# Performance work log

Hardware: AMD Instinct MI355X
Metric: run time of the kernel (lower is better)

The kernel has to match this reference:

```python
import jax, jax.numpy as jnp
import numpy as np


def _mlp3(x, w0, b0, w1, b1, w2, b2):
    x = jax.nn.relu(x @ w0.T + b0)
    x = jax.nn.relu(x @ w1.T + b1)
    return x @ w2.T + b2


def setup_inputs() -> dict:
    key = jax.random.key(0)
    ks = jax.random.split(key, 32)
    B, T, C, E, H, A = 64, 256, 53, 64, 64, 128
    C2 = C * C
    s = 0.1  # weight scale for numerical stability
    inp = {
        'x': jax.random.normal(ks[0], (B, T, C), jnp.float32),
        'w_emb': s * jax.random.normal(ks[1], (E, 1), jnp.float32),
        'b_emb': s * jax.random.normal(ks[2], (E,), jnp.float32),
        'w_ih': s * jax.random.normal(ks[3], (3 * H, E), jnp.float32),
        'w_hh': s * jax.random.normal(ks[4], (3 * H, H), jnp.float32),
        'b_ih': s * jax.random.normal(ks[5], (3 * H,), jnp.float32),
        'b_hh': s * jax.random.normal(ks[6], (3 * H,), jnp.float32),
        'q_w0': s * jax.random.normal(ks[7], (A, H), jnp.float32),
        'q_b0': s * jax.random.normal(ks[8], (A,), jnp.float32),
        'q_w1': s * jax.random.normal(ks[9], (A, A), jnp.float32),
        'q_b1': s * jax.random.normal(ks[10], (A,), jnp.float32),
        'q_w2': s * jax.random.normal(ks[11], (A, A), jnp.float32),
        'q_b2': s * jax.random.normal(ks[12], (A,), jnp.float32),
        'k_w0': s * jax.random.normal(ks[13], (A, H), jnp.float32),
        'k_b0': s * jax.random.normal(ks[14], (A,), jnp.float32),
        'k_w1': s * jax.random.normal(ks[15], (A, A), jnp.float32),
        'k_b1': s * jax.random.normal(ks[16], (A,), jnp.float32),
        'k_w2': s * jax.random.normal(ks[17], (A, A), jnp.float32),
        'k_b2': s * jax.random.normal(ks[18], (A,), jnp.float32),
        'gate_bias': jax.random.normal(ks[19], (C, C), jnp.float32),
        'pred_w': s * jax.random.normal(ks[20], (1, H), jnp.float32),
        'pred_b': s * jax.random.normal(ks[21], (1,), jnp.float32),
        'clf_w0': 0.02 * jax.random.normal(ks[22], (C2 // 2, C2), jnp.float32),
        'clf_b0': s * jax.random.normal(ks[23], (C2 // 2,), jnp.float32),
        'clf_w1': 0.02 * jax.random.normal(ks[24], (C2 // 4, C2 // 2), jnp.float32),
        'clf_b1': s * jax.random.normal(ks[25], (C2 // 4,), jnp.float32),
        'clf_w2': 0.02 * jax.random.normal(ks[26], (2, C2 // 4), jnp.float32),
        'clf_b2': s * jax.random.normal(ks[27], (2,), jnp.float32),
    }
    return inp


def reference(x, w_emb, b_emb, w_ih, w_hh, b_ih, b_hh,
              q_w0, q_b0, q_w1, q_b1, q_w2, q_b2,
              k_w0, k_b0, k_w1, k_b1, k_w2, k_b2,
              gate_bias, pred_w, pred_b,
              clf_w0, clf_b0, clf_w1, clf_b1, clf_w2, clf_b2):
    B, T, C = x.shape
    H = w_hh.shape[1]
    # single_embed Linear(1, E): embedded[b,t,c,e] = x[b,t,c]*w[e] + b[e]
    embedded = x[..., None] * w_emb[:, 0] + b_emb          # (B,T,C,E)
    emb_t = jnp.transpose(embedded, (1, 0, 2, 3))           # (T,B,C,E)
    h0 = jnp.zeros((B, C, H), x.dtype)

    def step(h, e_t):
        # GRU cell over B*C independent sequences (vectorized as (B,C,*))
        gi = e_t @ w_ih.T + b_ih                            # (B,C,3H)
        gh = h @ w_hh.T + b_hh
        ir, iz, inn = jnp.split(gi, 3, axis=-1)
        hr, hz, hn = jnp.split(gh, 3, axis=-1)
        r = jax.nn.sigmoid(ir + hr)
        z = jax.nn.sigmoid(iz + hz)
        n = jnp.tanh(inn + r * hn)
        h_gru = (1.0 - z) * n + z * h                       # (B,C,H)
        # gated self-attention mixing across components
        q = _mlp3(h_gru, q_w0, q_b0, q_w1, q_b1, q_w2, q_b2)
        k = _mlp3(h_gru, k_w0, k_b0, k_w1, k_b1, k_w2, k_b2)
        transfer = jnp.einsum('bch,bdh->bcd', q, k)         # (B,C,C)
        norms = jnp.sqrt(jnp.sum(transfer * transfer, axis=(1, 2), keepdims=True))
        transfer = transfer / norms                         # Frobenius matrix-norm divide
        gate = jax.nn.sigmoid(jnp.abs(transfer) + gate_bias)
        transfer = transfer * gate
        h_new = jnp.einsum('bcd,bdh->bch', transfer, h_gru)
        return h_new, (h_new, transfer)

    _, (hs, mix) = jax.lax.scan(step, h0, emb_t)
    hs = jnp.transpose(hs, (1, 0, 2, 3))                    # (B,T,C,H)
    mix = jnp.transpose(mix, (1, 0, 2, 3))                  # (B,T,C,C)

    hidden = hs[:, :-1]                                     # (B,T-1,C,H)
    predicted = (hidden @ pred_w.T + pred_b)[..., 0]        # (B,T-1,C)

    clf_in = mix.reshape(B, T, -1)                          # (B,T,C^2)
    mean_FNC = jnp.mean(clf_in, axis=1).reshape(B, C, C)
    z1 = jax.nn.relu(clf_in @ clf_w0.T + clf_b0)            # dropout is identity (eval)
    z2 = jax.nn.relu(z1 @ clf_w1.T + clf_b1)
    logits = jnp.mean(z2 @ clf_w2.T + clf_b2, axis=1)       # (B,2)
    return (logits, mean_FNC, mix, predicted, x[:, 1:, :])
```

## Files before the change

kernel.cpp:

```cpp
#include <hip/hip_runtime.h>
#include <hip/hip_fp16.h>

typedef _Float16 f16;
typedef f16 f16x4 __attribute__((ext_vector_type(4)));
typedef f16 f16x8 __attribute__((ext_vector_type(8)));
typedef float f32x4 __attribute__((ext_vector_type(4)));
typedef float f32x4u __attribute__((ext_vector_type(4), aligned(4)));

#define DEVINL __device__ __forceinline__
#define MFMA16(a, b, c) __builtin_amdgcn_mfma_f32_16x16x32_f16(a, b, c, 0, 0, 0)

#define BARRIER_LDS() asm volatile("s_waitcnt lgkmcnt(0)\n\ts_barrier" ::: "memory")

DEVINL float sigmoidf_(float v) { return 1.f / (1.f + __expf(-v)); }


__global__ __launch_bounds__(512)
void scan_kernel(const float* __restrict__ x,
                 const float* __restrict__ w_emb,
                 const float* __restrict__ b_emb,
                 const float* __restrict__ w_ih,
                 const float* __restrict__ w_hh,
                 const float* __restrict__ b_ih,
                 const float* __restrict__ b_hh,
                 const float* __restrict__ qw0, const float* __restrict__ qb0,
                 const float* __restrict__ qw1, const float* __restrict__ qb1,
                 const float* __restrict__ qw2, const float* __restrict__ qb2,
                 const float* __restrict__ kw0, const float* __restrict__ kb0,
                 const float* __restrict__ kw1, const float* __restrict__ kb1,
                 const float* __restrict__ kw2, const float* __restrict__ kb2,
                 const float* __restrict__ gate_bias,
                 const float* __restrict__ pred_w,
                 const float* __restrict__ pred_b,
                 float* __restrict__ out_meanF,
                 float* __restrict__ out_mix,
                 float* __restrict__ out_pred,
                 float* __restrict__ out_xcopy)
{
    __shared__ __align__(16) unsigned char smem[64900];
    float* hh  = (float*)smem;
    f16*   hK  = (f16*)(smem + 15232);
    f16*   hC  = (f16*)(smem + 23424);
    f16*   qk0 = (f16*)(smem + 31616);
    f16*   qk1 = (f16*)(smem + 48000);
    f16*   gh  = (f16*)(smem + 31616);
    f16*   trK = (f16*)(smem + 31616);
    float* xc  = (float*)(smem + 64384);
    float* pw  = (float*)(smem + 64608);
    float* red = (float*)(smem + 64864);

    const int b    = blockIdx.x;
    const int tid  = threadIdx.x;
    const int wv   = tid >> 6;
    const int lane = tid & 63;
    const int quad = lane >> 4;
    const int l15  = lane & 15;
    const int colg = (wv << 3) + (lane >> 3);
    const int rsub = lane & 7;

#define FRAG(buf, kt, nt) ((buf) + ((((kt) * 4 + (nt)) * 64 + lane) * 8))

    for (int i = tid; i < 56 * 68; i += 512) hh[i] = 0.f;
    for (int i = tid; i < 4096; i += 512) { hK[i] = (f16)0.f; hC[i] = (f16)0.f; }
    if (tid < 56) xc[tid] = 0.f;
    if (tid < 64) pw[tid] = pred_w[tid];

    float a_r = 0.f, a_z = 0.f, a_n = 0.f, s_r = 0.f, s_z = 0.f, s_n = 0.f;
    for (int e = 0; e < 64; e++) {
        float we = w_emb[e], be = b_emb[e];
        float w0 = w_ih[colg * 64 + e];
        float w1 = w_ih[(64 + colg) * 64 + e];
        float w2 = w_ih[(128 + colg) * 64 + e];
        a_r += w0 * we; s_r += w0 * be;
        a_z += w1 * we; s_z += w1 * be;
        a_n += w2 * we; s_n += w2 * be;
    }
    const float c_r = s_r + b_ih[colg] + b_hh[colg];
    const float c_z = s_z + b_ih[64 + colg] + b_hh[64 + colg];
    const float c_n = s_n + b_ih[128 + colg];
    const float bhn = b_hh[128 + colg];
    const float pb  = pred_b[0];

    auto ldfrag = [&](const float* W, int K, int mt, int kt) -> f16x8 {
        const float* p = W + (size_t)(mt * 16 + l15) * K + kt * 32 + quad * 8;
        float4 u0 = *(const float4*)p;
        float4 u1 = *(const float4*)(p + 4);
        f16x8 a;
        a[0] = (f16)u0.x; a[1] = (f16)u0.y; a[2] = (f16)u0.z; a[3] = (f16)u0.w;
        a[4] = (f16)u1.x; a[5] = (f16)u1.y; a[6] = (f16)u1.z; a[7] = (f16)u1.w;
        return a;
    };

    const int mtLo = (6 * wv) >> 2, mtHi = (6 * wv + 5) >> 2;
    f16x8 wg0k0 = ldfrag(w_hh, 64, mtLo, 0), wg0k1 = ldfrag(w_hh, 64, mtLo, 1);
    f16x8 wg1k0 = ldfrag(w_hh, 64, mtHi, 0), wg1k1 = ldfrag(w_hh, 64, mtHi, 1);

    f16x8 wq0f[2], wk0f[2], wq1f[4], wq2f[4], wk1f[4], wk2f[4];
#pragma unroll
    for (int kt = 0; kt < 2; kt++) {
        wq0f[kt] = ldfrag(qw0, 64, wv, kt);
        wk0f[kt] = ldfrag(kw0, 64, wv, kt);
    }
#pragma unroll
    for (int kt = 0; kt < 4; kt++) {
        wq1f[kt] = ldfrag(qw1, 128, wv, kt);
        wq2f[kt] = ldfrag(qw2, 128, wv, kt);
        wk1f[kt] = ldfrag(kw1, 128, wv, kt);
        wk2f[kt] = ldfrag(kw2, 128, wv, kt);
    }

    const int f0 = wv * 16 + quad * 4;
    f32x4 bq0v, bq1v, bq2v, bk0v, bk1v, bk2v;
#pragma unroll
    for (int r = 0; r < 4; r++) {
        bq0v[r] = qb0[f0 + r]; bq1v[r] = qb1[f0 + r]; bq2v[r] = qb2[f0 + r];
        bk0v[r] = kb0[f0 + r]; bk1v[r] = kb1[f0 + r]; bk2v[r] = kb2[f0 + r];
    }

    const int tmt = wv & 3, tnt0 = (wv >> 2) * 2;
    float gbv[8], mf[8];
#pragma unroll
    for (int i = 0; i < 2; i++)
#pragma unroll
        for (int r = 0; r < 4; r++) {
            int c = tmt * 16 + quad * 4 + r, d = (tnt0 + i) * 16 + l15;
            gbv[i * 4 + r] = (c < 53 && d < 53) ? gate_bias[c * 53 + d] : 0.f;
            mf[i * 4 + r] = 0.f;
        }

    auto cwrite = [&](f16* dst, int ct, const f32x4 acc, const f32x4 bv, bool rel) {
        const int kts  = wv >> 1;
        const int sub  = (2 * wv + (quad >> 1)) & 3;
        const int base = ((kts * 4 + ct) * 64 + (l15 + 16 * sub)) * 8 + (quad & 1) * 4;
        f16x4 pk;
#pragma unroll
        for (int r = 0; r < 4; r++) {
            float v = acc[r] + bv[r];
            if (rel) v = fmaxf(v, 0.f);
            pk[r] = (f16)v;
        }
        *(f16x4*)(dst + base) = pk;
    };

    __syncthreads();

    f16x8 bf[4][4];

#define PRELOAD(SRC) do { \
    _Pragma("unroll") for (int ct = 0; ct < 4; ct++) \
        _Pragma("unroll") for (int kt = 0; kt < 4; kt++) \
            bf[ct][kt] = *(const f16x8*)FRAG(SRC, kt, ct); } while (0)

#define MLP4(WF, DST, BV, REL) do { \
    f32x4 a0 = {0.f,0.f,0.f,0.f}, a1 = {0.f,0.f,0.f,0.f}; \
    f32x4 a2 = {0.f,0.f,0.f,0.f}, a3 = {0.f,0.f,0.f,0.f}; \
    _Pragma("unroll") for (int kt = 0; kt < 4; kt++) { \
        a0 = MFMA16(WF[kt], bf[0][kt], a0); \
        a1 = MFMA16(WF[kt], bf[1][kt], a1); \
        a2 = MFMA16(WF[kt], bf[2][kt], a2); \
        a3 = MFMA16(WF[kt], bf[3][kt], a3); } \
    cwrite(DST, 0, a0, BV, REL); cwrite(DST, 1, a1, BV, REL); \
    cwrite(DST, 2, a2, BV, REL); cwrite(DST, 3, a3, BV, REL); } while (0)

    float xv = 0.f;
    if (tid < 53) xv = x[(size_t)b * 256 * 53 + tid];

    for (int t = 0; t < 256; t++) {
        if (tid < 53) xc[tid] = xv;
        {
#pragma unroll
            for (int i = 0; i < 6; i++) {
                int tau = 6 * wv + i, mt = tau >> 2, ct = tau & 3;
                bool hi = (mt != mtLo);
                f32x4 acc = {0.f, 0.f, 0.f, 0.f};
                acc = MFMA16(hi ? wg1k0 : wg0k0, *(const f16x8*)FRAG(hK, 0, ct), acc);
                acc = MFMA16(hi ? wg1k1 : wg0k1, *(const f16x8*)FRAG(hK, 1, ct), acc);
                int gbase = (mt * 16 + quad * 4) * 68 + ct * 16 + l15;
#pragma unroll
                for (int r = 0; r < 4; r++) gh[gbase + r * 68] = (f16)acc[r];
            }
        }
        BARRIER_LDS();
        {
#pragma unroll
            for (int r = 0; r < 7; r++) {
                int c = rsub + 8 * r;
                float hr = (float)gh[colg * 68 + c];
                float hz = (float)gh[(64 + colg) * 68 + c];
                float hn = (float)gh[(128 + colg) * 68 + c];
                float xcv = xc[c];
                float hp = hh[c * 68 + colg];
                float rr = sigmoidf_(xcv * a_r + c_r + hr);
                float zz = sigmoidf_(xcv * a_z + c_z + hz);
                float e2 = __expf(2.f * (xcv * a_n + c_n + rr * (hn + bhn)));
                float nn = 1.f - 2.f / (e2 + 1.f);
                float hg = (1.f - zz) * nn + zz * hp;
                hh[c * 68 + colg] = hg;
                f16 h6 = (f16)hg;
                hK[(((colg >> 5) * 4 + (c >> 4)) * 64 + (c & 15) + 16 * ((colg >> 3) & 3)) * 8 + (colg & 7)] = h6;
                hC[(((c >> 5) * 4 + (colg >> 4)) * 64 + (colg & 15) + 16 * ((c >> 3) & 3)) * 8 + (c & 7)] = h6;
            }
        }
        BARRIER_LDS();
        {
            if (tid < 53) {
                if (t >= 1) out_xcopy[((size_t)b * 255 + (t - 1)) * 53 + tid] = xv;
                if (t < 255) xv = x[((size_t)b * 256 + t + 1) * 53 + tid];
            }
            f32x4 a0 = {0.f,0.f,0.f,0.f}, a1 = {0.f,0.f,0.f,0.f};
            f32x4 a2 = {0.f,0.f,0.f,0.f}, a3 = {0.f,0.f,0.f,0.f};
#pragma unroll
            for (int kt = 0; kt < 2; kt++) {
                a0 = MFMA16(wq0f[kt], *(const f16x8*)FRAG(hK, kt, 0), a0);
                a1 = MFMA16(wq0f[kt], *(const f16x8*)FRAG(hK, kt, 1), a1);
                a2 = MFMA16(wq0f[kt], *(const f16x8*)FRAG(hK, kt, 2), a2);
                a3 = MFMA16(wq0f[kt], *(const f16x8*)FRAG(hK, kt, 3), a3);
            }
            cwrite(qk0, 0, a0, bq0v, true); cwrite(qk0, 1, a1, bq0v, true);
            cwrite(qk0, 2, a2, bq0v, true); cwrite(qk0, 3, a3, bq0v, true);
            f32x4 k0 = {0.f,0.f,0.f,0.f}, k1 = {0.f,0.f,0.f,0.f};
            f32x4 k2 = {0.f,0.f,0.f,0.f}, k3 = {0.f,0.f,0.f,0.f};
#pragma unroll
            for (int kt = 0; kt < 2; kt++) {
                k0 = MFMA16(wk0f[kt], *(const f16x8*)FRAG(hK, kt, 0), k0);
                k1 = MFMA16(wk0f[kt], *(const f16x8*)FRAG(hK, kt, 1), k1);
                k2 = MFMA16(wk0f[kt], *(const f16x8*)FRAG(hK, kt, 2), k2);
                k3 = MFMA16(wk0f[kt], *(const f16x8*)FRAG(hK, kt, 3), k3);
            }
            cwrite(qk1, 0, k0, bk0v, true); cwrite(qk1, 1, k1, bk0v, true);
            cwrite(qk1, 2, k2, bk0v, true); cwrite(qk1, 3, k3, bk0v, true);
        }
        BARRIER_LDS();
        PRELOAD(qk0);
        BARRIER_LDS();
        MLP4(wq1f, qk0, bq1v, true);
        PRELOAD(qk1);
        BARRIER_LDS();
        MLP4(wk1f, qk1, bk1v, true);
        PRELOAD(qk0);
        BARRIER_LDS();
        MLP4(wq2f, qk0, bq2v, false);
        PRELOAD(qk1);
        BARRIER_LDS();
        MLP4(wk2f, qk1, bk2v, false);
        BARRIER_LDS();
        f32x4 tacc0 = {0.f,0.f,0.f,0.f}, tacc1 = {0.f,0.f,0.f,0.f};
        {
            f16x8 qa[4];
#pragma unroll
            for (int kt = 0; kt < 4; kt++) qa[kt] = *(const f16x8*)FRAG(qk0, kt, tmt);
#pragma unroll
            for (int kt = 0; kt < 4; kt++) {
                tacc0 = MFMA16(qa[kt], *(const f16x8*)FRAG(qk1, kt, tnt0), tacc0);
                tacc1 = MFMA16(qa[kt], *(const f16x8*)FRAG(qk1, kt, tnt0 + 1), tacc1);
            }
            float ssq = 0.f;
#pragma unroll
            for (int r = 0; r < 4; r++) {
                int c = tmt * 16 + quad * 4 + r;
                if (c < 53) {
                    if (tnt0 * 16 + l15 < 53)       ssq += tacc0[r] * tacc0[r];
                    if ((tnt0 + 1) * 16 + l15 < 53) ssq += tacc1[r] * tacc1[r];
                }
            }
#pragma unroll
            for (int off = 32; off > 0; off >>= 1) ssq += __shfl_down(ssq, off);
            if (lane == 0) red[wv] = ssq;
        }
        BARRIER_LDS();
        float ov[8];
        {
            float s2 = 0.f;
#pragma unroll
            for (int w8 = 0; w8 < 8; w8++) s2 += red[w8];
            const float inv = rsqrtf(s2);
#pragma unroll
            for (int i = 0; i < 2; i++)
#pragma unroll
                for (int r = 0; r < 4; r++) {
                    int c = tmt * 16 + quad * 4 + r;
                    int d = (tnt0 + i) * 16 + l15;
                    float v = (i == 0 ? tacc0[r] : tacc1[r]) * inv;
                    float g = sigmoidf_(fabsf(v) + gbv[i * 4 + r]);
                    v *= g;
                    bool ok = (c < 53) & (d < 53);
                    v = ok ? v : 0.f;
                    ov[i * 4 + r] = v;
                    mf[i * 4 + r] += v;
                    trK[(((d >> 5) * 4 + (c >> 4)) * 64 + (c & 15) + 16 * ((d >> 3) & 3)) * 8 + (d & 7)] = (f16)v;
                }
        }
        BARRIER_LDS();
        {
            const size_t mixbase = ((size_t)b * 256 + t) * 2809;
#pragma unroll
            for (int i = 0; i < 2; i++)
#pragma unroll
                for (int r = 0; r < 4; r++) {
                    int c = tmt * 16 + quad * 4 + r;
                    int d = (tnt0 + i) * 16 + l15;
                    if ((c < 53) & (d < 53)) out_mix[mixbase + c * 53 + d] = ov[i * 4 + r];
                }
        }
        {
            f32x4 h0 = {0.f,0.f,0.f,0.f}, h1 = {0.f,0.f,0.f,0.f};
            f16x8 ta0 = *(const f16x8*)FRAG(trK, 0, tmt);
            f16x8 ta1 = *(const f16x8*)FRAG(trK, 1, tmt);
            h0 = MFMA16(ta0, *(const f16x8*)FRAG(hC, 0, tnt0), h0);
            h0 = MFMA16(ta1, *(const f16x8*)FRAG(hC, 1, tnt0), h0);
            h1 = MFMA16(ta0, *(const f16x8*)FRAG(hC, 0, tnt0 + 1), h1);
            h1 = MFMA16(ta1, *(const f16x8*)FRAG(hC, 1, tnt0 + 1), h1);
#pragma unroll
            for (int i = 0; i < 2; i++)
#pragma unroll
                for (int r = 0; r < 4; r++) {
                    int c = tmt * 16 + quad * 4 + r;
                    int e = (tnt0 + i) * 16 + l15;
                    float v = (i == 0 ? h0[r] : h1[r]);
                    if (c < 56) hh[c * 68 + e] = v;
                    hK[(((e >> 5) * 4 + (c >> 4)) * 64 + (c & 15) + 16 * ((e >> 3) & 3)) * 8 + (e & 7)] = (f16)v;
                }
        }
        BARRIER_LDS();
        if (t < 255 && tid < 53) {
            const float* hrow = hh + tid * 68;
            float s = pb;
#pragma unroll 4
            for (int e4 = 0; e4 < 16; e4++) {
                float4 hv = *(const float4*)(hrow + e4 * 4);
                float4 wv4 = *(const float4*)(pw + e4 * 4);
                s += hv.x * wv4.x + hv.y * wv4.y + hv.z * wv4.z + hv.w * wv4.w;
            }
            out_pred[((size_t)b * 255 + t) * 53 + tid] = s;
        }
    }

#pragma unroll
    for (int i = 0; i < 2; i++)
#pragma unroll
        for (int r = 0; r < 4; r++) {
            int c = tmt * 16 + quad * 4 + r;
            int d = (tnt0 + i) * 16 + l15;
            if (c < 53 && d < 53)
                out_meanF[(size_t)b * 2809 + c * 53 + d] = mf[i * 4 + r] * (1.f / 256.f);
        }
#undef FRAG
#undef PRELOAD
#undef MLP4
}

DEVINL void cvt16(const float* p, f16x8& lo, f16x8& hi) {
    f32x4u u0 = *(const f32x4u*)p;
    f32x4u u1 = *(const f32x4u*)(p + 4);
    f32x4u u2 = *(const f32x4u*)(p + 8);
    f32x4u u3 = *(const f32x4u*)(p + 12);
    lo[0] = (f16)u0.x; lo[1] = (f16)u0.y; lo[2] = (f16)u0.z; lo[3] = (f16)u0.w;
    lo[4] = (f16)u1.x; lo[5] = (f16)u1.y; lo[6] = (f16)u1.z; lo[7] = (f16)u1.w;
    hi[0] = (f16)u2.x; hi[1] = (f16)u2.y; hi[2] = (f16)u2.z; hi[3] = (f16)u2.w;
    hi[4] = (f16)u3.x; hi[5] = (f16)u3.y; hi[6] = (f16)u3.z; hi[7] = (f16)u3.w;
}

template<bool AHALF, bool COLSUM>
__global__ __launch_bounds__(256)
void clf_mfma(const void* __restrict__ Ap,
              const float* __restrict__ W,
              const float* __restrict__ bias,
              __half* __restrict__ z_out,
              float* __restrict__ colsum_out,
              int N, int K, int lda, int Kpad, int ldz)
{
    __shared__ __align__(16) f16 As[4096];
    __shared__ __align__(16) f16 Bs[4096];

    const int tid  = threadIdx.x;
    const int wv   = tid >> 6;
    const int lane = tid & 63;
    const int quad = lane >> 4;
    const int l15  = lane & 15;
    const int wm   = wv & 1;
    const int wn   = wv >> 1;
    const int m0   = blockIdx.x * 128;
    const int n0   = blockIdx.y * 128;

    const int srow = tid >> 1;
    const int skh  = (tid & 1) * 16;
    const int sdst = ((srow >> 4) * 64 + (skh >> 3) * 16 + (srow & 15)) * 8;

    f32x4 acc[4][4];
#pragma unroll
    for (int i = 0; i < 4; i++)
#pragma unroll
        for (int j = 0; j < 4; j++)
            acc[i][j] = (f32x4){0.f, 0.f, 0.f, 0.f};

    for (int k0 = 0; k0 < Kpad; k0 += 32) {
        {
            f16x8 lo, hi;
            if constexpr (AHALF) {
                const f16* p = (const f16*)Ap + (size_t)(m0 + srow) * lda + k0 + skh;
                lo = *(const f16x8*)p;
                hi = *(const f16x8*)(p + 8);
            } else {
                const float* p = (const float*)Ap + (size_t)(m0 + srow) * lda + k0 + skh;
                if (k0 + 32 <= K) {
                    cvt16(p, lo, hi);
                } else {
                    int kr = K - (k0 + skh);
#pragma unroll
                    for (int j = 0; j < 8; j++) lo[j] = (f16)((j < kr) ? p[j] : 0.f);
#pragma unroll
                    for (int j = 0; j < 8; j++) hi[j] = (f16)((j + 8 < kr) ? p[j + 8] : 0.f);
                }
            }
            *(f16x8*)(As + sdst)       = lo;
            *(f16x8*)(As + sdst + 128) = hi;
        }
        {
            f16x8 lo, hi;
#pragma unroll
            for (int j = 0; j < 8; j++) { lo[j] = (f16)0.f; hi[j] = (f16)0.f; }
            const int nrow = n0 + srow;
            if (nrow < N) {
                const float* p = W + (size_t)nrow * K + k0 + skh;
                if (k0 + 32 <= K) {
                    cvt16(p, lo, hi);
                } else {
                    int kr = K - (k0 + skh);
#pragma unroll
                    for (int j = 0; j < 8; j++) lo[j] = (f16)((j < kr) ? p[j] : 0.f);
#pragma unroll
                    for (int j = 0; j < 8; j++) hi[j] = (f16)((j + 8 < kr) ? p[j + 8] : 0.f);
                }
            }
            *(f16x8*)(Bs + sdst)       = lo;
            *(f16x8*)(Bs + sdst + 128) = hi;
        }
        __syncthreads();
        {
            f16x8 afr[4], bfr[4];
#pragma unroll
            for (int i = 0; i < 4; i++)
                afr[i] = *(const f16x8*)(As + ((wm * 4 + i) * 64 + lane) * 8);
#pragma unroll
            for (int i = 0; i < 4; i++)
                bfr[i] = *(const f16x8*)(Bs + ((wn * 4 + i) * 64 + lane) * 8);
#pragma unroll
            for (int mi = 0; mi < 4; mi++)
#pragma unroll
                for (int ni = 0; ni < 4; ni++)
                    acc[mi][ni] = MFMA16(afr[mi], bfr[ni], acc[mi][ni]);
        }
        __syncthreads();
    }

    if constexpr (!COLSUM) {
#pragma unroll
        for (int ni = 0; ni < 4; ni++) {
            int n = n0 + wn * 64 + ni * 16 + l15;
            float bj = (n < N) ? bias[n] : 0.f;
#pragma unroll
            for (int mi = 0; mi < 4; mi++) {
                int m = m0 + wm * 64 + mi * 16 + quad * 4;
#pragma unroll
                for (int r = 0; r < 4; r++) {
                    float v = (n < N) ? fmaxf(acc[mi][ni][r] + bj, 0.f) : 0.f;
                    z_out[(size_t)(m + r) * ldz + n] = __float2half(v);
                }
            }
        }
    } else {
        const int batch = m0 >> 8;
#pragma unroll
        for (int ni = 0; ni < 4; ni++) {
            int n = n0 + wn * 64 + ni * 16 + l15;
            float bj = (n < N) ? bias[n] : 0.f;
            float s = 0.f;
#pragma unroll
            for (int mi = 0; mi < 4; mi++)
#pragma unroll
                for (int r = 0; r < 4; r++)
                    s += fmaxf(acc[mi][ni][r] + bj, 0.f);
            s += __shfl_down(s, 32);
            s += __shfl_down(s, 16);
            if (quad == 0 && n < N)
                atomicAdd(&colsum_out[batch * 704 + n], s);
        }
    }
}

__global__ __launch_bounds__(128)
void logits_kernel(const float* __restrict__ zsum,
                   const float* __restrict__ w2,
                   const float* __restrict__ b2,
                   float* __restrict__ out)
{
    int tid = threadIdx.x;
    int bb = tid >> 1, o = tid & 1;
    const float* zs = zsum + bb * 704;
    const float* wrow = w2 + o * 702;
    float s = 0.f;
    for (int j = 0; j < 702; j++) s += zs[j] * wrow[j];
    out[bb * 2 + o] = s * (1.f / 256.f) + b2[o];
}

extern "C" void kernel_launch(void* const* d_in, const int* in_sizes, int n_in,
                              void* d_out, int out_size, void* d_ws, size_t ws_size,
                              hipStream_t stream)
{
    const float* x      = (const float*)d_in[0];
    const float* w_emb  = (const float*)d_in[1];
    const float* b_emb  = (const float*)d_in[2];
    const float* w_ih   = (const float*)d_in[3];
    const float* w_hh   = (const float*)d_in[4];
    const float* b_ih   = (const float*)d_in[5];
    const float* b_hh   = (const float*)d_in[6];
    const float* qw0 = (const float*)d_in[7];
    const float* qb0 = (const float*)d_in[8];
    const float* qw1 = (const float*)d_in[9];
    const float* qb1 = (const float*)d_in[10];
    const float* qw2 = (const float*)d_in[11];
    const float* qb2 = (const float*)d_in[12];
    const float* kw0 = (const float*)d_in[13];
    const float* kb0 = (const float*)d_in[14];
    const float* kw1 = (const float*)d_in[15];
    const float* kb1 = (const float*)d_in[16];
    const float* kw2 = (const float*)d_in[17];
    const float* kb2 = (const float*)d_in[18];
    const float* gate_bias = (const float*)d_in[19];
    const float* pred_w = (const float*)d_in[20];
    const float* pred_b = (const float*)d_in[21];
    const float* cw0 = (const float*)d_in[22];
    const float* cb0 = (const float*)d_in[23];
    const float* cw1 = (const float*)d_in[24];
    const float* cb1 = (const float*)d_in[25];
    const float* cw2 = (const float*)d_in[26];
    const float* cb2 = (const float*)d_in[27];

    float* out_logits = (float*)d_out;
    float* out_meanF  = (float*)d_out + 128;
    float* out_mix    = (float*)d_out + 128 + 179776;
    float* out_pred   = out_mix + 46022656;
    float* out_xcopy  = out_pred + 864960;

    float*  zsum = (float*)d_ws;
    __half* z1   = (__half*)((char*)d_ws + (1 << 18));

    hipMemsetAsync(zsum, 0, 64 * 704 * sizeof(float), stream);

    scan_kernel<<<64, 512, 0, stream>>>(
        x, w_emb, b_emb, w_ih, w_hh, b_ih, b_hh,
        qw0, qb0, qw1, qb1, qw2, qb2,
        kw0, kb0, kw1, kb1, kw2, kb2,
        gate_bias, pred_w, pred_b,
        out_meanF, out_mix, out_pred, out_xcopy);

    clf_mfma<false, false><<<dim3(128, 11), 256, 0, stream>>>(
        out_mix, cw0, cb0, z1, nullptr, 1404, 2809, 2809, 2816, 1408);

    clf_mfma<true, true><<<dim3(128, 6), 256, 0, stream>>>(
        z1, cw1, cb1, nullptr, zsum, 702, 1404, 1408, 1408, 0);

    logits_kernel<<<1, 128, 0, stream>>>(zsum, cw2, cb2, out_logits);
}
```

Baseline: 3.103 ms.

## Emit fp16 padded mix copy from scan and register-prefetch GEMM tiles

The scan kernel now also writes an fp16 copy of the mix matrix into workspace, padded to a 2816-element row stride with zeroed tail columns. When the workspace is large enough, the first classifier GEMM reads this half-precision copy with aligned vector loads instead of converting fp32 mix rows. The GEMM kernel also gains a software pipeline that loads the next K-tile into registers while the current tile is computed, and swaps __syncthreads for an lgkmcnt wait plus barrier. The cost is extra global writes in the serial scan kernel and a larger workspace requirement.

```diff
diff --git a/kernel.cpp b/kernel.cpp
--- a/kernel.cpp
+++ b/kernel.cpp
@@ -35,7 +35,8 @@
                  float* __restrict__ out_meanF,
                  float* __restrict__ out_mix,
                  float* __restrict__ out_pred,
-                 float* __restrict__ out_xcopy)
+                 float* __restrict__ out_xcopy,
+                 f16* __restrict__ out_mixh)
 {
     __shared__ __align__(16) unsigned char smem[64900];
     float* hh  = (float*)smem;
@@ -64,6 +65,12 @@
     for (int i = tid; i < 4096; i += 512) { hK[i] = (f16)0.f; hC[i] = (f16)0.f; }
     if (tid < 56) xc[tid] = 0.f;
     if (tid < 64) pw[tid] = pred_w[tid];
+    if (out_mixh) {
+        for (int i = tid; i < 256 * 7; i += 512) {
+            int row = b * 256 + i / 7, cc = 2809 + i % 7;
+            out_mixh[(size_t)row * 2816 + cc] = (f16)0.f;
+        }
+    }
 
     float a_r = 0.f, a_z = 0.f, a_n = 0.f, s_r = 0.f, s_z = 0.f, s_n = 0.f;
     for (int e = 0; e < 64; e++) {
@@ -293,13 +300,18 @@
         BARRIER_LDS();
         {
             const size_t mixbase = ((size_t)b * 256 + t) * 2809;
+            const size_t mhbase  = ((size_t)b * 256 + t) * 2816;
 #pragma unroll
             for (int i = 0; i < 2; i++)
 #pragma unroll
                 for (int r = 0; r < 4; r++) {
                     int c = tmt * 16 + quad * 4 + r;
                     int d = (tnt0 + i) * 16 + l15;
-                    if ((c < 53) & (d < 53)) out_mix[mixbase + c * 53 + d] = ov[i * 4 + r];
+                    if ((c < 53) & (d < 53)) {
+                        float v = ov[i * 4 + r];
+                        out_mix[mixbase + c * 53 + d] = v;
+                        if (out_mixh) out_mixh[mhbase + c * 53 + d] = (f16)v;
+                    }
                 }
         }
         {
@@ -347,17 +359,6 @@
 #undef FRAG
 #undef PRELOAD
 #undef MLP4
-}
-
-DEVINL void cvt16(const float* p, f16x8& lo, f16x8& hi) {
-    f32x4u u0 = *(const f32x4u*)p;
-    f32x4u u1 = *(const f32x4u*)(p + 4);
-    f32x4u u2 = *(const f32x4u*)(p + 8);
-    f32x4u u3 = *(const f32x4u*)(p + 12);
-    lo[0] = (f16)u0.x; lo[1] = (f16)u0.y; lo[2] = (f16)u0.z; lo[3] = (f16)u0.w;
-    lo[4] = (f16)u1.x; lo[5] = (f16)u1.y; lo[6] = (f16)u1.z; lo[7] = (f16)u1.w;
-    hi[0] = (f16)u2.x; hi[1] = (f16)u2.y; hi[2] = (f16)u2.z; hi[3] = (f16)u2.w;
-    hi[4] = (f16)u3.x; hi[5] = (f16)u3.y; hi[6] = (f16)u3.z; hi[7] = (f16)u3.w;
 }
 
 template<bool AHALF, bool COLSUM>
@@ -385,6 +386,8 @@
     const int srow = tid >> 1;
     const int skh  = (tid & 1) * 16;
     const int sdst = ((srow >> 4) * 64 + (skh >> 3) * 16 + (srow & 15)) * 8;
+    const int nrow = n0 + srow;
+    const bool bok = (nrow < N);
 
     f32x4 acc[4][4];
 #pragma unroll
@@ -393,49 +396,73 @@
         for (int j = 0; j < 4; j++)
             acc[i][j] = (f32x4){0.f, 0.f, 0.f, 0.f};
 
-    for (int k0 = 0; k0 < Kpad; k0 += 32) {
-        {
+    f16x8 pa0, pa1;
+    float fa[16];
+    float fb[16];
+
+    auto issueA = [&](int k0) {
+        if constexpr (AHALF) {
+            const f16* p = (const f16*)Ap + (size_t)(m0 + srow) * lda + k0 + skh;
+            pa0 = *(const f16x8*)p;
+            pa1 = *(const f16x8*)(p + 8);
+        } else {
+            const float* p = (const float*)Ap + (size_t)(m0 + srow) * lda + k0 + skh;
+            if (k0 + 32 <= K) {
+#pragma unroll
+                for (int q4 = 0; q4 < 4; q4++) {
+                    f32x4u u = *(const f32x4u*)(p + q4 * 4);
+                    fa[q4 * 4] = u[0]; fa[q4 * 4 + 1] = u[1];
+                    fa[q4 * 4 + 2] = u[2]; fa[q4 * 4 + 3] = u[3];
+                }
+            } else {
+#pragma unroll
+                for (int j = 0; j < 16; j++) {
+                    int k = k0 + skh + j;
+                    fa[j] = (k < K) ? p[j] : 0.f;
+                }
+            }
+        }
+    };
+    auto issueB = [&](int k0) {
+        const float* p = W + (size_t)nrow * K + k0 + skh;
+        if (bok && k0 + 32 <= K) {
+#pragma unroll
+            for (int q4 = 0; q4 < 4; q4++) {
+                f32x4u u = *(const f32x4u*)(p + q4 * 4);
+                fb[q4 * 4] = u[0]; fb[q4 * 4 + 1] = u[1];
+                fb[q4 * 4 + 2] = u[2]; fb[q4 * 4 + 3] = u[3];
+            }
+        } else {
+#pragma unroll
+            for (int j = 0; j < 16; j++) {
+                int k = k0 + skh + j;
+                fb[j] = (bok && k < K) ? p[j] : 0.f;
+            }
+        }
+    };
+    auto stage = [&]() {
+        if constexpr (AHALF) {
+            *(f16x8*)(As + sdst)       = pa0;
+            *(f16x8*)(As + sdst + 128) = pa1;
+        } else {
             f16x8 lo, hi;
-            if constexpr (AHALF) {
-                const f16* p = (const f16*)Ap + (size_t)(m0 + srow) * lda + k0 + skh;
-                lo = *(const f16x8*)p;
-                hi = *(const f16x8*)(p + 8);
-            } else {
-                const float* p = (const float*)Ap + (size_t)(m0 + srow) * lda + k0 + skh;
-                if (k0 + 32 <= K) {
-                    cvt16(p, lo, hi);
-                } else {
-                    int kr = K - (k0 + skh);
-#pragma unroll
-                    for (int j = 0; j < 8; j++) lo[j] = (f16)((j < kr) ? p[j] : 0.f);
-#pragma unroll
-                    for (int j = 0; j < 8; j++) hi[j] = (f16)((j + 8 < kr) ? p[j + 8] : 0.f);
-                }
-            }
+#pragma unroll
+            for (int j = 0; j < 8; j++) { lo[j] = (f16)fa[j]; hi[j] = (f16)fa[j + 8]; }
             *(f16x8*)(As + sdst)       = lo;
             *(f16x8*)(As + sdst + 128) = hi;
         }
-        {
-            f16x8 lo, hi;
-#pragma unroll
-            for (int j = 0; j < 8; j++) { lo[j] = (f16)0.f; hi[j] = (f16)0.f; }
-            const int nrow = n0 + srow;
-            if (nrow < N) {
-                const float* p = W + (size_t)nrow * K + k0 + skh;
-                if (k0 + 32 <= K) {
-                    cvt16(p, lo, hi);
-                } else {
-                    int kr = K - (k0 + skh);
-#pragma unroll
-                    for (int j = 0; j < 8; j++) lo[j] = (f16)((j < kr) ? p[j] : 0.f);
-#pragma unroll
-                    for (int j = 0; j < 8; j++) hi[j] = (f16)((j + 8 < kr) ? p[j + 8] : 0.f);
-                }
-            }
-            *(f16x8*)(Bs + sdst)       = lo;
-            *(f16x8*)(Bs + sdst + 128) = hi;
-        }
-        __syncthreads();
+        f16x8 blo, bhi;
+#pragma unroll
+        for (int j = 0; j < 8; j++) { blo[j] = (f16)fb[j]; bhi[j] = (f16)fb[j + 8]; }
+        *(f16x8*)(Bs + sdst)       = blo;
+        *(f16x8*)(Bs + sdst + 128) = bhi;
+    };
+
+    issueA(0); issueB(0);
+    for (int k0 = 0; k0 < Kpad; k0 += 32) {
+        stage();
+        if (k0 + 32 < Kpad) { issueA(k0 + 32); issueB(k0 + 32); }
+        BARRIER_LDS();
         {
             f16x8 afr[4], bfr[4];
 #pragma unroll
@@ -450,7 +477,7 @@
                 for (int ni = 0; ni < 4; ni++)
                     acc[mi][ni] = MFMA16(afr[mi], bfr[ni], acc[mi][ni]);
         }
-        __syncthreads();
+        BARRIER_LDS();
     }
 
     if constexpr (!COLSUM) {
@@ -544,6 +571,10 @@
 
     float*  zsum = (float*)d_ws;
     __half* z1   = (__half*)((char*)d_ws + (1 << 18));
+    const size_t mixh_off  = (size_t)(1 << 18) + 46137344;
+    const size_t mixh_need = mixh_off + (size_t)16384 * 2816 * 2;
+    const bool useh = (ws_size >= mixh_need);
+    f16* mixh = useh ? (f16*)((char*)d_ws + mixh_off) : nullptr;
 
     hipMemsetAsync(zsum, 0, 64 * 704 * sizeof(float), stream);
 
@@ -552,10 +583,15 @@
         qw0, qb0, qw1, qb1, qw2, qb2,
         kw0, kb0, kw1, kb1, kw2, kb2,
         gate_bias, pred_w, pred_b,
-        out_meanF, out_mix, out_pred, out_xcopy);
-
-    clf_mfma<false, false><<<dim3(128, 11), 256, 0, stream>>>(
-        out_mix, cw0, cb0, z1, nullptr, 1404, 2809, 2809, 2816, 1408);
+        out_meanF, out_mix, out_pred, out_xcopy, mixh);
+
+    if (useh) {
+        clf_mfma<true, false><<<dim3(128, 11), 256, 0, stream>>>(
+            mixh, cw0, cb0, z1, nullptr, 1404, 2809, 2816, 2816, 1408);
+    } else {
+        clf_mfma<false, false><<<dim3(128, 11), 256, 0, stream>>>(
+            out_mix, cw0, cb0, z1, nullptr, 1404, 2809, 2809, 2816, 1408);
+    }
 
     clf_mfma<true, true><<<dim3(128, 6), 256, 0, stream>>>(
         z1, cw1, cb1, nullptr, zsum, 702, 1404, 1408, 1408, 0);
```

New measurement: 2.984 ms. 3.8% less time.
